# Kernel optimization log

Measured on AMD Instinct MI355X. Metric: run time of the kernel, lower is better.

## Reference

```python
import jax, jax.numpy as jnp
import numpy as np

D = 1024
H = 16
HD = D // H
B = 8
S = 1024


def setup_inputs() -> dict:
    key = jax.random.key(0)
    ks = jax.random.split(key, 12)
    std = 0.02
    inp = {
        "x": jax.random.normal(ks[0], (B, S, D), jnp.float32),
        "rel_pos_enc": jax.random.normal(ks[1], (S, HD), jnp.float32) * std,
        "attention_mask": jax.random.randint(ks[2], (B, S), 0, 2, jnp.int32),
        "Wq": jax.random.normal(ks[3], (D, D), jnp.float32) * std,
        "bq": jnp.zeros((D,), jnp.float32),
        "Wk": jax.random.normal(ks[4], (D, D), jnp.float32) * std,
        "bk": jnp.zeros((D,), jnp.float32),
        "Wv": jax.random.normal(ks[5], (D, D), jnp.float32) * std,
        "bv": jnp.zeros((D,), jnp.float32),
        "Wo": jax.random.normal(ks[6], (D, D), jnp.float32) * std,
        "bo": jnp.zeros((D,), jnp.float32),
    }
    return inp


def reference(x, rel_pos_enc, attention_mask, Wq, bq, Wk, bk, Wv, bv, Wo, bo):
    b, s, d = x.shape
    scale = HD ** -0.5
    # projections + split heads -> [B, H, S, hd]
    q = (x @ Wq + bq).reshape(b, s, H, HD).transpose(0, 2, 1, 3)
    k = (x @ Wk + bk).reshape(b, s, H, HD).transpose(0, 2, 1, 3)
    v = (x @ Wv + bv).reshape(b, s, H, HD).transpose(0, 2, 1, 3)
    # content scores [B,H,S,S]
    scores = jnp.einsum("bhsd,bhtd->bhst", q, k) * scale
    # additive relative-position bias: q . rel_pos_enc[t]  -> [B,H,S,S]
    scores = scores + jnp.einsum("bhsd,td->bhst", q, rel_pos_enc)
    # key-padding mask [B,S] -> [B,1,1,S]
    scores = jnp.where(attention_mask[:, None, None, :] == 0, -jnp.inf, scores)
    attn = jax.nn.softmax(scores, axis=-1)
    ctx = jnp.einsum("bhst,bhtd->bhsd", attn, v)
    ctx = ctx.transpose(0, 2, 1, 3).reshape(b, s, d)
    return ctx @ Wo + bo
```

## Files before the change

kernel.cpp:

```cpp
#include <hip/hip_runtime.h>

#define DD 1024
#define HH 16
#define HDD 64
#define BBATCH 8
#define SS 1024
#define NROW (BBATCH*SS)
#define PSTR 72

typedef _Float16 f16x8 __attribute__((ext_vector_type(8)));
typedef _Float16 f16x4 __attribute__((ext_vector_type(4)));
typedef float    f32x4 __attribute__((ext_vector_type(4)));

__device__ __forceinline__ void async_cp16(const void* g, void* l) {
    __builtin_amdgcn_global_load_lds(
        (const __attribute__((address_space(1))) void*)g,
        (__attribute__((address_space(3))) void*)l, 16, 0, 0);
}

__global__ __launch_bounds__(256) void conv_x_kernel(
    const float* __restrict__ x, _Float16* __restrict__ xh)
{
    size_t i8 = ((size_t)blockIdx.x * 256 + threadIdx.x) * 8;
    float4 v0 = *(const float4*)&x[i8];
    float4 v1 = *(const float4*)&x[i8 + 4];
    float vf[8] = {v0.x, v0.y, v0.z, v0.w, v1.x, v1.y, v1.z, v1.w};
    f16x8 hv;
    #pragma unroll
    for (int c = 0; c < 8; c++) hv[c] = (_Float16)vf[c];
    *(f16x8*)&xh[i8] = hv;
}

__global__ __launch_bounds__(256) void conv_w_kernel(
    const float* __restrict__ Wq, const float* __restrict__ Wk,
    const float* __restrict__ Wv, const float* __restrict__ Wo,
    _Float16* __restrict__ wt, _Float16* __restrict__ wot)
{
    __shared__ float T[64][65];
    const int z = blockIdx.z;
    const float* src = (z == 0) ? Wq : (z == 1) ? Wk : (z == 2) ? Wv : Wo;
    _Float16* dh = (z < 3) ? wt + (size_t)z * 1024 * 1024 : wot;
    const int k0 = blockIdx.x * 64, n0 = blockIdx.y * 64;
    const int tid = threadIdx.x;

    #pragma unroll
    for (int rep = 0; rep < 4; rep++) {
        int e = rep * 256 + tid;
        int kr = e >> 4, nc = (e & 15) * 4;
        *(float4*)&T[kr][nc] = *(const float4*)&src[(size_t)(k0 + kr) * 1024 + n0 + nc];
    }
    __syncthreads();
    #pragma unroll
    for (int rep = 0; rep < 4; rep++) {
        int e = rep * 256 + tid;
        int nr = e >> 4, kc = (e & 15) * 4;
        f16x4 hv;
        #pragma unroll
        for (int c = 0; c < 4; c++) hv[c] = (_Float16)T[kc + c][nr];
        *(f16x4*)&dh[(size_t)(n0 + nr) * 1024 + k0 + kc] = hv;
    }
}

__global__ __launch_bounds__(256) void gemm_f16(
    const _Float16* __restrict__ Ag, const _Float16* __restrict__ Bg,
    const float* __restrict__ b0, const float* __restrict__ b1,
    const float* __restrict__ b2, const float* __restrict__ rel,
    _Float16* __restrict__ oq, _Float16* __restrict__ okh,
    _Float16* __restrict__ ovt, float* __restrict__ dOut, int mode)
{
    __shared__ _Float16 smem[32768];

    const int tid = threadIdx.x;
    const int w = tid >> 6, l = tid & 63;
    const int lane15 = l & 15, quad = l >> 4;
    const int rm = (w >> 1) * 64, cn = (w & 1) * 64;
    const size_t r0 = (size_t)blockIdx.y * 128;
    const size_t n0 = (size_t)blockIdx.x * 128;

    const int srow = tid >> 3;
    const int schp = tid & 7;
    const int sch  = schp ^ (srow & 7);

    f32x4 acc[4][4] = {};

    #pragma unroll
    for (int i = 0; i < 4; i++) {
        int row = i * 32 + srow;
        int s = row * 8 + schp;
        async_cp16(&Ag[(r0 + row) * 1024 + sch * 8], &smem[s * 8]);
        async_cp16(&Bg[(n0 + row) * 1024 + sch * 8], &smem[8192 + s * 8]);
    }
    #pragma unroll
    for (int i = 0; i < 4; i++) {
        int row = i * 32 + srow;
        int s = row * 8 + schp;
        async_cp16(&Ag[(r0 + row) * 1024 + 64 + sch * 8], &smem[16384 + s * 8]);
        async_cp16(&Bg[(n0 + row) * 1024 + 64 + sch * 8], &smem[16384 + 8192 + s * 8]);
    }

    for (int ks = 0; ks < 16; ks++) {
        const _Float16* Ah = smem + (ks & 1) * 16384;
        const _Float16* Bh = Ah + 8192;

        if (ks < 15) asm volatile("s_waitcnt vmcnt(8)" ::: "memory");
        else         asm volatile("s_waitcnt vmcnt(0)" ::: "memory");
        __builtin_amdgcn_sched_barrier(0);
        __builtin_amdgcn_s_barrier();
        __builtin_amdgcn_sched_barrier(0);

        #pragma unroll
        for (int ksub = 0; ksub < 2; ksub++) {
            f16x8 ah[4], bh4[4];
            #pragma unroll
            for (int ii = 0; ii < 4; ii++) {
                int row = rm + ii * 16 + lane15;
                int chp = (ksub * 4 + quad) ^ (row & 7);
                ah[ii] = *(const f16x8*)&Ah[row * 64 + chp * 8];
            }
            #pragma unroll
            for (int jj = 0; jj < 4; jj++) {
                int col = cn + jj * 16 + lane15;
                int chp = (ksub * 4 + quad) ^ (col & 7);
                bh4[jj] = *(const f16x8*)&Bh[col * 64 + chp * 8];
            }
            #pragma unroll
            for (int ii = 0; ii < 4; ii++)
                #pragma unroll
                for (int jj = 0; jj < 4; jj++)
                    acc[ii][jj] = __builtin_amdgcn_mfma_f32_16x16x32_f16(
                        ah[ii], bh4[jj], acc[ii][jj], 0, 0, 0);
        }

        __builtin_amdgcn_sched_barrier(0);
        __builtin_amdgcn_s_barrier();
        __builtin_amdgcn_sched_barrier(0);

        if (ks + 2 < 16) {
            const int kb = (ks + 2) * 64;
            _Float16* An = smem + (ks & 1) * 16384;
            _Float16* Bn = An + 8192;
            #pragma unroll
            for (int i = 0; i < 4; i++) {
                int row = i * 32 + srow;
                int s = row * 8 + schp;
                async_cp16(&Ag[(r0 + row) * 1024 + kb + sch * 8], &An[s * 8]);
                async_cp16(&Bg[(n0 + row) * 1024 + kb + sch * 8], &Bn[s * 8]);
            }
        }
    }

    if (mode == 0) {
        const int z = blockIdx.x >> 3;
        const float* bias = (z == 0) ? b0 : (z == 1) ? b1 : b2;
        const int nbase = (blockIdx.x & 7) * 128 + cn;
        #pragma unroll
        for (int ii = 0; ii < 4; ii++)
            #pragma unroll
            for (int jj = 0; jj < 4; jj++) {
                int nc = nbase + jj * 16 + lane15;
                int hh = nc >> 6, hd = nc & 63;
                float bsv = bias[nc];
                #pragma unroll
                for (int r = 0; r < 4; r++) {
                    int gr = (int)r0 + rm + ii * 16 + quad * 4 + r;
                    int bb = gr >> 10, s = gr & 1023;
                    float val = acc[ii][jj][r] + bsv;
                    size_t hidx = (((size_t)bb * HH + hh) * SS + s) * HDD + hd;
                    if (z == 0) {
                        oq[hidx] = (_Float16)val;
                    } else if (z == 1) {
                        okh[hidx] = (_Float16)(val * 0.125f + rel[s * HDD + hd]);
                    } else {
                        ovt[(((size_t)bb * HH + hh) * HDD + hd) * SS + s] = (_Float16)val;
                    }
                }
            }
    } else {
        #pragma unroll
        for (int ii = 0; ii < 4; ii++)
            #pragma unroll
            for (int jj = 0; jj < 4; jj++) {
                int nc = (int)n0 + cn + jj * 16 + lane15;
                float bsv = b0[nc];
                #pragma unroll
                for (int r = 0; r < 4; r++) {
                    int gr = (int)r0 + rm + ii * 16 + quad * 4 + r;
                    dOut[(size_t)gr * DD + nc] = acc[ii][jj][r] + bsv;
                }
            }
    }
}

__global__ __launch_bounds__(512, 4) void attn_mfma(
    const _Float16* __restrict__ qh, const _Float16* __restrict__ kh,
    const _Float16* __restrict__ vt, const int* __restrict__ mask,
    _Float16* __restrict__ ctx)
{
    __shared__ _Float16 Kbuf[2][64 * PSTR];
    __shared__ _Float16 Vbuf[2][64 * PSTR];
    __shared__ _Float16 Ps[128 * PSTR];
    __shared__ float maddL[1024];

    const int tid = threadIdx.x;
    const int w = tid >> 6, l = tid & 63;
    const int lane15 = l & 15, quad = l >> 4;
    const int id = blockIdx.x;
    const int qt = id >> 7;
    const int bh = id & 127;
    const int b = bh >> 4, h = bh & 15;
    const size_t kbase0 = (size_t)bh * SS;
    const size_t vbase0 = (size_t)bh * HDD;
    const int qrow_blk = qt * 128 + w * 16;

    for (int i = tid; i < 1024; i += 512)
        maddL[i] = (mask[b * SS + i] == 0) ? -1e30f : 0.0f;

    f16x8 qf[2];
    #pragma unroll
    for (int ks = 0; ks < 2; ks++)
        qf[ks] = *(const f16x8*)&qh[(kbase0 + qrow_blk + lane15) * HDD + ks * 32 + quad * 8];

    f16x8 vone;
    #pragma unroll
    for (int j = 0; j < 8; j++) vone[j] = (lane15 == 0) ? (_Float16)1.0f : (_Float16)0.0f;

    f32x4 O[5] = {};

    const int grow = tid >> 3;
    const int gcc  = (tid & 7) * 8;
    const _Float16* kp = &kh[(kbase0 + grow) * HDD + gcc];
    const _Float16* vp = &vt[(vbase0 + grow) * SS + gcc];
    f16x8 kreg = *(const f16x8*)kp;
    f16x8 vreg = *(const f16x8*)vp;

    int p = 0;
    for (int kt = 0; kt < 16; kt++) {
        *(f16x8*)&Kbuf[p][grow * PSTR + gcc] = kreg;
        *(f16x8*)&Vbuf[p][grow * PSTR + gcc] = vreg;
        __syncthreads();

        const int nkt = (kt + 1) & 15;
        kreg = *(const f16x8*)(kp + (size_t)nkt * 64 * HDD);
        vreg = *(const f16x8*)(vp + (size_t)nkt * 64);

        const int t0 = kt * 64;

        f32x4 S[4];
        #pragma unroll
        for (int nt = 0; nt < 4; nt++) {
            f16x8 kf0 = *(const f16x8*)&Kbuf[p][(nt * 16 + lane15) * PSTR + quad * 8];
            f16x8 kf1 = *(const f16x8*)&Kbuf[p][(nt * 16 + lane15) * PSTR + 32 + quad * 8];
            f32x4 c = {};
            c = __builtin_amdgcn_mfma_f32_16x16x32_f16(qf[0], kf0, c, 0, 0, 0);
            c = __builtin_amdgcn_mfma_f32_16x16x32_f16(qf[1], kf1, c, 0, 0, 0);
            S[nt] = c;
        }

        const int rowb = w * 16 + quad * 4;
        #pragma unroll
        for (int nt = 0; nt < 4; nt++) {
            float madd = maddL[t0 + nt * 16 + lane15] - 3.0f;
            int colp = (nt * 16 + lane15 + 16 * quad) & 63;
            #pragma unroll
            for (int r = 0; r < 4; r++)
                Ps[(rowb + r) * PSTR + colp] = (_Float16)__expf(S[nt][r] + madd);
        }

        const int swz = 16 * (lane15 >> 2);
        #pragma unroll
        for (int ks2 = 0; ks2 < 2; ks2++) {
            int colp = (ks2 * 32 + quad * 8 + swz) & 63;
            f16x8 pf = *(const f16x8*)&Ps[(w * 16 + lane15) * PSTR + colp];
            #pragma unroll
            for (int nd = 0; nd < 4; nd++) {
                f16x8 vf = *(const f16x8*)&Vbuf[p][(nd * 16 + lane15) * PSTR + ks2 * 32 + quad * 8];
                O[nd] = __builtin_amdgcn_mfma_f32_16x16x32_f16(pf, vf, O[nd], 0, 0, 0);
            }
            O[4] = __builtin_amdgcn_mfma_f32_16x16x32_f16(pf, vone, O[4], 0, 0, 0);
        }
        p ^= 1;
    }

    float linv[4];
    #pragma unroll
    for (int r = 0; r < 4; r++) {
        float lsum = __shfl(O[4][r], l & 48, 64);
        linv[r] = 1.0f / lsum;
    }
    #pragma unroll
    for (int nd = 0; nd < 4; nd++) {
        int d = nd * 16 + lane15;
        #pragma unroll
        for (int r = 0; r < 4; r++) {
            int qrow = qt * 128 + w * 16 + quad * 4 + r;
            ctx[((size_t)b * SS + qrow) * DD + h * HDD + d] =
                (_Float16)(O[nd][r] * linv[r]);
        }
    }
}

extern "C" void kernel_launch(void* const* d_in, const int* in_sizes, int n_in,
                              void* d_out, int out_size, void* d_ws, size_t ws_size,
                              hipStream_t stream) {
    const float* x    = (const float*)d_in[0];
    const float* rel  = (const float*)d_in[1];
    const int*   mask = (const int*)d_in[2];
    const float* Wq = (const float*)d_in[3];  const float* bq = (const float*)d_in[4];
    const float* Wk = (const float*)d_in[5];  const float* bk = (const float*)d_in[6];
    const float* Wv = (const float*)d_in[7];  const float* bv = (const float*)d_in[8];
    const float* Wo = (const float*)d_in[9];  const float* bo = (const float*)d_in[10];
    float* out = (float*)d_out;

    const size_t XN = (size_t)NROW * DD;
    char* p = (char*)d_ws;
    _Float16* xh  = (_Float16*)p; p += XN * 2;
    _Float16* wt  = (_Float16*)p; p += (size_t)3072 * 1024 * 2;
    _Float16* wot = (_Float16*)p; p += (size_t)1024 * 1024 * 2;
    _Float16* qhp = (_Float16*)p; p += XN * 2;
    _Float16* khp = (_Float16*)p; p += XN * 2;
    _Float16* vtp = (_Float16*)p; p += XN * 2;
    _Float16* ctx = xh;

    conv_x_kernel<<<dim3((unsigned)(XN / 2048)), 256, 0, stream>>>(x, xh);
    conv_w_kernel<<<dim3(16, 16, 4), 256, 0, stream>>>(Wq, Wk, Wv, Wo, wt, wot);
    gemm_f16<<<dim3(24, 64), 256, 0, stream>>>(
        xh, wt, bq, bk, bv, rel, qhp, khp, vtp, nullptr, 0);
    attn_mfma<<<dim3(1024), 512, 0, stream>>>(
        qhp, khp, vtp, mask, ctx);
    gemm_f16<<<dim3(8, 64), 256, 0, stream>>>(
        ctx, wot, bo, nullptr, nullptr, nullptr,
        nullptr, nullptr, nullptr, out, 1);
}
```

Baseline: 289.7 us.

## Load K/V fragments directly from global memory and remap GEMM workgroups across XCDs

The attention kernel drops its shared-memory double-buffered K/V staging and per-tile barriers, so each wave reads its MFMA operand fragments straight from global memory and relies on L2/cache for reuse across the 8 waves. The GEMM remaps workgroup IDs so consecutive tiles land on the same XCD chunk, which is meant to improve L2 locality. This removes barrier and LDS traffic but multiplies global or L2 loads per block and exposes load latency that the prefetch used to hide. A barrier is added after the mask fill.

After: 450.3 us. +55.4%, slower.

```diff
diff --git a/kernel.cpp b/kernel.cpp
--- a/kernel.cpp
+++ b/kernel.cpp
@@ -74,8 +74,16 @@
     const int w = tid >> 6, l = tid & 63;
     const int lane15 = l & 15, quad = l >> 4;
     const int rm = (w >> 1) * 64, cn = (w & 1) * 64;
-    const size_t r0 = (size_t)blockIdx.y * 128;
-    const size_t n0 = (size_t)blockIdx.x * 128;
+
+    const int nwg = (int)(gridDim.x * gridDim.y);
+    const int chunk = nwg >> 3;
+    const int orig = (int)(blockIdx.y * gridDim.x + blockIdx.x);
+    const int wgid = (orig & 7) * chunk + (orig >> 3);
+    const int bx = wgid % (int)gridDim.x;
+    const int by = wgid / (int)gridDim.x;
+
+    const size_t r0 = (size_t)by * 128;
+    const size_t n0 = (size_t)bx * 128;
 
     const int srow = tid >> 3;
     const int schp = tid & 7;
@@ -150,9 +158,9 @@
     }
 
     if (mode == 0) {
-        const int z = blockIdx.x >> 3;
+        const int z = bx >> 3;
         const float* bias = (z == 0) ? b0 : (z == 1) ? b1 : b2;
-        const int nbase = (blockIdx.x & 7) * 128 + cn;
+        const int nbase = (bx & 7) * 128 + cn;
         #pragma unroll
         for (int ii = 0; ii < 4; ii++)
             #pragma unroll
@@ -196,8 +204,6 @@
     const _Float16* __restrict__ vt, const int* __restrict__ mask,
     _Float16* __restrict__ ctx)
 {
-    __shared__ _Float16 Kbuf[2][64 * PSTR];
-    __shared__ _Float16 Vbuf[2][64 * PSTR];
     __shared__ _Float16 Ps[128 * PSTR];
     __shared__ float maddL[1024];
 
@@ -214,6 +220,7 @@
 
     for (int i = tid; i < 1024; i += 512)
         maddL[i] = (mask[b * SS + i] == 0) ? -1e30f : 0.0f;
+    __syncthreads();
 
     f16x8 qf[2];
     #pragma unroll
@@ -226,30 +233,18 @@
 
     f32x4 O[5] = {};
 
-    const int grow = tid >> 3;
-    const int gcc  = (tid & 7) * 8;
-    const _Float16* kp = &kh[(kbase0 + grow) * HDD + gcc];
-    const _Float16* vp = &vt[(vbase0 + grow) * SS + gcc];
-    f16x8 kreg = *(const f16x8*)kp;
-    f16x8 vreg = *(const f16x8*)vp;
-
-    int p = 0;
+    const _Float16* kfrag = &kh[(kbase0 + lane15) * HDD + quad * 8];
+    const _Float16* vfrag = &vt[(vbase0 + lane15) * SS + quad * 8];
+
     for (int kt = 0; kt < 16; kt++) {
-        *(f16x8*)&Kbuf[p][grow * PSTR + gcc] = kreg;
-        *(f16x8*)&Vbuf[p][grow * PSTR + gcc] = vreg;
-        __syncthreads();
-
-        const int nkt = (kt + 1) & 15;
-        kreg = *(const f16x8*)(kp + (size_t)nkt * 64 * HDD);
-        vreg = *(const f16x8*)(vp + (size_t)nkt * 64);
-
         const int t0 = kt * 64;
 
         f32x4 S[4];
         #pragma unroll
         for (int nt = 0; nt < 4; nt++) {
-            f16x8 kf0 = *(const f16x8*)&Kbuf[p][(nt * 16 + lane15) * PSTR + quad * 8];
-            f16x8 kf1 = *(const f16x8*)&Kbuf[p][(nt * 16 + lane15) * PSTR + 32 + quad * 8];
+            const _Float16* kp = kfrag + (size_t)(t0 + nt * 16) * HDD;
+            f16x8 kf0 = *(const f16x8*)kp;
+            f16x8 kf1 = *(const f16x8*)(kp + 32);
             f32x4 c = {};
             c = __builtin_amdgcn_mfma_f32_16x16x32_f16(qf[0], kf0, c, 0, 0, 0);
             c = __builtin_amdgcn_mfma_f32_16x16x32_f16(qf[1], kf1, c, 0, 0, 0);
@@ -273,12 +268,11 @@
             f16x8 pf = *(const f16x8*)&Ps[(w * 16 + lane15) * PSTR + colp];
             #pragma unroll
             for (int nd = 0; nd < 4; nd++) {
-                f16x8 vf = *(const f16x8*)&Vbuf[p][(nd * 16 + lane15) * PSTR + ks2 * 32 + quad * 8];
+                f16x8 vf = *(const f16x8*)(vfrag + (size_t)(nd * 16) * SS + t0 + ks2 * 32);
                 O[nd] = __builtin_amdgcn_mfma_f32_16x16x32_f16(pf, vf, O[nd], 0, 0, 0);
             }
             O[4] = __builtin_amdgcn_mfma_f32_16x16x32_f16(pf, vone, O[4], 0, 0, 0);
         }
-        p ^= 1;
     }
 
     float linv[4];
```

## Process two query row groups per wave to reuse K/V tiles in attention

Applied to the files above, without the earlier changes.

Each wave now handles 32 query rows (two 16-row groups) instead of 16, so each block covers 256 query rows and the grid is halved to 512 blocks. K and V tiles loaded into shared memory, and the K/V fragments read from it, are reused across both row groups, which halves global and LDS traffic for K/V per query. The cost is more registers for the doubled accumulators, a larger P buffer in shared memory, and fewer blocks to fill the GPU.

Result: faster. 277.9 us (-4.1%).

```diff
diff --git a/kernel.cpp b/kernel.cpp
--- a/kernel.cpp
+++ b/kernel.cpp
@@ -198,7 +198,7 @@
 {
     __shared__ _Float16 Kbuf[2][64 * PSTR];
     __shared__ _Float16 Vbuf[2][64 * PSTR];
-    __shared__ _Float16 Ps[128 * PSTR];
+    __shared__ _Float16 Ps[256 * PSTR];
     __shared__ float maddL[1024];
 
     const int tid = threadIdx.x;
@@ -210,21 +210,23 @@
     const int b = bh >> 4, h = bh & 15;
     const size_t kbase0 = (size_t)bh * SS;
     const size_t vbase0 = (size_t)bh * HDD;
-    const int qrow_blk = qt * 128 + w * 16;
+    const int qrow_blk = qt * 256 + w * 32;
 
     for (int i = tid; i < 1024; i += 512)
         maddL[i] = (mask[b * SS + i] == 0) ? -1e30f : 0.0f;
 
-    f16x8 qf[2];
-    #pragma unroll
-    for (int ks = 0; ks < 2; ks++)
-        qf[ks] = *(const f16x8*)&qh[(kbase0 + qrow_blk + lane15) * HDD + ks * 32 + quad * 8];
+    f16x8 qf[2][2];
+    #pragma unroll
+    for (int g = 0; g < 2; g++)
+        #pragma unroll
+        for (int ks = 0; ks < 2; ks++)
+            qf[g][ks] = *(const f16x8*)&qh[(kbase0 + qrow_blk + g * 16 + lane15) * HDD + ks * 32 + quad * 8];
 
     f16x8 vone;
     #pragma unroll
     for (int j = 0; j < 8; j++) vone[j] = (lane15 == 0) ? (_Float16)1.0f : (_Float16)0.0f;
 
-    f32x4 O[5] = {};
+    f32x4 O[2][5] = {};
 
     const int grow = tid >> 3;
     const int gcc  = (tid & 7) * 8;
@@ -245,56 +247,59 @@
 
         const int t0 = kt * 64;
 
-        f32x4 S[4];
         #pragma unroll
         for (int nt = 0; nt < 4; nt++) {
             f16x8 kf0 = *(const f16x8*)&Kbuf[p][(nt * 16 + lane15) * PSTR + quad * 8];
             f16x8 kf1 = *(const f16x8*)&Kbuf[p][(nt * 16 + lane15) * PSTR + 32 + quad * 8];
-            f32x4 c = {};
-            c = __builtin_amdgcn_mfma_f32_16x16x32_f16(qf[0], kf0, c, 0, 0, 0);
-            c = __builtin_amdgcn_mfma_f32_16x16x32_f16(qf[1], kf1, c, 0, 0, 0);
-            S[nt] = c;
-        }
-
-        const int rowb = w * 16 + quad * 4;
-        #pragma unroll
-        for (int nt = 0; nt < 4; nt++) {
             float madd = maddL[t0 + nt * 16 + lane15] - 3.0f;
             int colp = (nt * 16 + lane15 + 16 * quad) & 63;
             #pragma unroll
-            for (int r = 0; r < 4; r++)
-                Ps[(rowb + r) * PSTR + colp] = (_Float16)__expf(S[nt][r] + madd);
+            for (int g = 0; g < 2; g++) {
+                f32x4 c = {};
+                c = __builtin_amdgcn_mfma_f32_16x16x32_f16(qf[g][0], kf0, c, 0, 0, 0);
+                c = __builtin_amdgcn_mfma_f32_16x16x32_f16(qf[g][1], kf1, c, 0, 0, 0);
+                int rowb = w * 32 + g * 16 + quad * 4;
+                #pragma unroll
+                for (int r = 0; r < 4; r++)
+                    Ps[(rowb + r) * PSTR + colp] = (_Float16)__expf(c[r] + madd);
+            }
         }
 
         const int swz = 16 * (lane15 >> 2);
         #pragma unroll
         for (int ks2 = 0; ks2 < 2; ks2++) {
             int colp = (ks2 * 32 + quad * 8 + swz) & 63;
-            f16x8 pf = *(const f16x8*)&Ps[(w * 16 + lane15) * PSTR + colp];
+            f16x8 pf0 = *(const f16x8*)&Ps[(w * 32 + lane15) * PSTR + colp];
+            f16x8 pf1 = *(const f16x8*)&Ps[(w * 32 + 16 + lane15) * PSTR + colp];
             #pragma unroll
             for (int nd = 0; nd < 4; nd++) {
                 f16x8 vf = *(const f16x8*)&Vbuf[p][(nd * 16 + lane15) * PSTR + ks2 * 32 + quad * 8];
-                O[nd] = __builtin_amdgcn_mfma_f32_16x16x32_f16(pf, vf, O[nd], 0, 0, 0);
-            }
-            O[4] = __builtin_amdgcn_mfma_f32_16x16x32_f16(pf, vone, O[4], 0, 0, 0);
+                O[0][nd] = __builtin_amdgcn_mfma_f32_16x16x32_f16(pf0, vf, O[0][nd], 0, 0, 0);
+                O[1][nd] = __builtin_amdgcn_mfma_f32_16x16x32_f16(pf1, vf, O[1][nd], 0, 0, 0);
+            }
+            O[0][4] = __builtin_amdgcn_mfma_f32_16x16x32_f16(pf0, vone, O[0][4], 0, 0, 0);
+            O[1][4] = __builtin_amdgcn_mfma_f32_16x16x32_f16(pf1, vone, O[1][4], 0, 0, 0);
         }
         p ^= 1;
     }
 
-    float linv[4];
-    #pragma unroll
-    for (int r = 0; r < 4; r++) {
-        float lsum = __shfl(O[4][r], l & 48, 64);
-        linv[r] = 1.0f / lsum;
-    }
-    #pragma unroll
-    for (int nd = 0; nd < 4; nd++) {
-        int d = nd * 16 + lane15;
+    #pragma unroll
+    for (int g = 0; g < 2; g++) {
+        float linv[4];
         #pragma unroll
         for (int r = 0; r < 4; r++) {
-            int qrow = qt * 128 + w * 16 + quad * 4 + r;
-            ctx[((size_t)b * SS + qrow) * DD + h * HDD + d] =
-                (_Float16)(O[nd][r] * linv[r]);
+            float lsum = __shfl(O[g][4][r], l & 48, 64);
+            linv[r] = 1.0f / lsum;
+        }
+        #pragma unroll
+        for (int nd = 0; nd < 4; nd++) {
+            int d = nd * 16 + lane15;
+            #pragma unroll
+            for (int r = 0; r < 4; r++) {
+                int qrow = qt * 256 + w * 32 + g * 16 + quad * 4 + r;
+                ctx[((size_t)b * SS + qrow) * DD + h * HDD + d] =
+                    (_Float16)(O[g][nd][r] * linv[r]);
+            }
         }
     }
 }
@@ -325,7 +330,7 @@
     conv_w_kernel<<<dim3(16, 16, 4), 256, 0, stream>>>(Wq, Wk, Wv, Wo, wt, wot);
     gemm_f16<<<dim3(24, 64), 256, 0, stream>>>(
         xh, wt, bq, bk, bv, rel, qhp, khp, vtp, nullptr, 0);
-    attn_mfma<<<dim3(1024), 512, 0, stream>>>(
+    attn_mfma<<<dim3(512), 512, 0, stream>>>(
         qhp, khp, vtp, mask, ctx);
     gemm_f16<<<dim3(8, 64), 256, 0, stream>>>(
         ctx, wot, bo, nullptr, nullptr, nullptr,
```

## Switch attention to 32x32 MFMA with register-resident P and 256-row query tiles

Applied to the files above, without the earlier changes.

The attention kernel now computes S transposed (K·Q) with 32x32x16 MFMA so the probability tile stays in registers. It is repacked across lane halves with shuffles instead of being round-tripped through shared memory. Row sums are accumulated in registers instead of through an extra MFMA against a ones vector, and the mask becomes a multiplicative fp16 array. Each block now handles 256 query rows with 32 rows per wave, halving the grid to 512 blocks, which raises register pressure and lowers the number of blocks per CU.

Result: faster. 280.5 us (-3.2%).

```diff
diff --git a/kernel.cpp b/kernel.cpp
--- a/kernel.cpp
+++ b/kernel.cpp
@@ -11,6 +11,8 @@
 typedef _Float16 f16x8 __attribute__((ext_vector_type(8)));
 typedef _Float16 f16x4 __attribute__((ext_vector_type(4)));
 typedef float    f32x4 __attribute__((ext_vector_type(4)));
+typedef float    f32x16 __attribute__((ext_vector_type(16)));
+typedef unsigned int u32x4 __attribute__((ext_vector_type(4)));
 
 __device__ __forceinline__ void async_cp16(const void* g, void* l) {
     __builtin_amdgcn_global_load_lds(
@@ -198,33 +200,30 @@
 {
     __shared__ _Float16 Kbuf[2][64 * PSTR];
     __shared__ _Float16 Vbuf[2][64 * PSTR];
-    __shared__ _Float16 Ps[128 * PSTR];
-    __shared__ float maddL[1024];
+    __shared__ _Float16 maskh[1024];
 
     const int tid = threadIdx.x;
     const int w = tid >> 6, l = tid & 63;
-    const int lane15 = l & 15, quad = l >> 4;
+    const int l31 = l & 31, hi = l >> 5;
     const int id = blockIdx.x;
     const int qt = id >> 7;
     const int bh = id & 127;
     const int b = bh >> 4, h = bh & 15;
     const size_t kbase0 = (size_t)bh * SS;
     const size_t vbase0 = (size_t)bh * HDD;
-    const int qrow_blk = qt * 128 + w * 16;
+    const int qbase = qt * 256 + w * 32;
 
     for (int i = tid; i < 1024; i += 512)
-        maddL[i] = (mask[b * SS + i] == 0) ? -1e30f : 0.0f;
-
-    f16x8 qf[2];
-    #pragma unroll
-    for (int ks = 0; ks < 2; ks++)
-        qf[ks] = *(const f16x8*)&qh[(kbase0 + qrow_blk + lane15) * HDD + ks * 32 + quad * 8];
-
-    f16x8 vone;
-    #pragma unroll
-    for (int j = 0; j < 8; j++) vone[j] = (lane15 == 0) ? (_Float16)1.0f : (_Float16)0.0f;
-
-    f32x4 O[5] = {};
+        maskh[i] = (_Float16)(mask[b * SS + i] != 0 ? 1.0f : 0.0f);
+
+    f16x8 qfrag[4];
+    #pragma unroll
+    for (int kc = 0; kc < 4; kc++)
+        qfrag[kc] = *(const f16x8*)&qh[(kbase0 + qbase + l31) * HDD + kc * 16 + hi * 8];
+
+    f32x16 O0 = {};
+    f32x16 O1 = {};
+    float rs = 0.0f;
 
     const int grow = tid >> 3;
     const int gcc  = (tid & 7) * 8;
@@ -233,10 +232,10 @@
     f16x8 kreg = *(const f16x8*)kp;
     f16x8 vreg = *(const f16x8*)vp;
 
-    int p = 0;
+    int pb = 0;
     for (int kt = 0; kt < 16; kt++) {
-        *(f16x8*)&Kbuf[p][grow * PSTR + gcc] = kreg;
-        *(f16x8*)&Vbuf[p][grow * PSTR + gcc] = vreg;
+        *(f16x8*)&Kbuf[pb][grow * PSTR + gcc] = kreg;
+        *(f16x8*)&Vbuf[pb][grow * PSTR + gcc] = vreg;
         __syncthreads();
 
         const int nkt = (kt + 1) & 15;
@@ -245,57 +244,65 @@
 
         const int t0 = kt * 64;
 
-        f32x4 S[4];
-        #pragma unroll
-        for (int nt = 0; nt < 4; nt++) {
-            f16x8 kf0 = *(const f16x8*)&Kbuf[p][(nt * 16 + lane15) * PSTR + quad * 8];
-            f16x8 kf1 = *(const f16x8*)&Kbuf[p][(nt * 16 + lane15) * PSTR + 32 + quad * 8];
-            f32x4 c = {};
-            c = __builtin_amdgcn_mfma_f32_16x16x32_f16(qf[0], kf0, c, 0, 0, 0);
-            c = __builtin_amdgcn_mfma_f32_16x16x32_f16(qf[1], kf1, c, 0, 0, 0);
-            S[nt] = c;
+        #pragma unroll
+        for (int T = 0; T < 2; T++) {
+            f32x16 S = {};
+            #pragma unroll
+            for (int kc = 0; kc < 4; kc++) {
+                f16x8 kf = *(const f16x8*)&Kbuf[pb][(T * 32 + l31) * PSTR + kc * 16 + hi * 8];
+                S = __builtin_amdgcn_mfma_f32_32x32x16_f16(kf, qfrag[kc], S, 0, 0, 0);
+            }
+
+            unsigned short phb[16];
+            #pragma unroll
+            for (int rq = 0; rq < 4; rq++) {
+                f16x4 mh = *(const f16x4*)&maskh[t0 + T * 32 + rq * 8 + hi * 4];
+                #pragma unroll
+                for (int dd = 0; dd < 4; dd++) {
+                    const int r = rq * 4 + dd;
+                    float e = __expf(S[r] - 3.0f) * (float)mh[dd];
+                    _Float16 eh = (_Float16)e;
+                    rs += (float)eh;
+                    phb[r] = *(unsigned short*)&eh;
+                }
+            }
+            unsigned pk[8];
+            #pragma unroll
+            for (int c = 0; c < 8; c++)
+                pk[c] = (unsigned)phb[2 * c] | ((unsigned)phb[2 * c + 1] << 16);
+
+            #pragma unroll
+            for (int ct = 0; ct < 2; ct++) {
+                unsigned s0 = hi ? pk[4 * ct + 0] : pk[4 * ct + 2];
+                unsigned s1 = hi ? pk[4 * ct + 1] : pk[4 * ct + 3];
+                unsigned r0 = (unsigned)__shfl_xor((int)s0, 32, 64);
+                unsigned r1 = (unsigned)__shfl_xor((int)s1, 32, 64);
+                u32x4 W;
+                W[0] = hi ? r0 : pk[4 * ct + 0];
+                W[1] = hi ? r1 : pk[4 * ct + 1];
+                W[2] = hi ? pk[4 * ct + 2] : r0;
+                W[3] = hi ? pk[4 * ct + 3] : r1;
+                f16x8 pf = __builtin_bit_cast(f16x8, W);
+
+                f16x8 vf0 = *(const f16x8*)&Vbuf[pb][(l31) * PSTR + T * 32 + ct * 16 + hi * 8];
+                O0 = __builtin_amdgcn_mfma_f32_32x32x16_f16(pf, vf0, O0, 0, 0, 0);
+                f16x8 vf1 = *(const f16x8*)&Vbuf[pb][(32 + l31) * PSTR + T * 32 + ct * 16 + hi * 8];
+                O1 = __builtin_amdgcn_mfma_f32_32x32x16_f16(pf, vf1, O1, 0, 0, 0);
+            }
         }
-
-        const int rowb = w * 16 + quad * 4;
-        #pragma unroll
-        for (int nt = 0; nt < 4; nt++) {
-            float madd = maddL[t0 + nt * 16 + lane15] - 3.0f;
-            int colp = (nt * 16 + lane15 + 16 * quad) & 63;
-            #pragma unroll
-            for (int r = 0; r < 4; r++)
-                Ps[(rowb + r) * PSTR + colp] = (_Float16)__expf(S[nt][r] + madd);
-        }
-
-        const int swz = 16 * (lane15 >> 2);
-        #pragma unroll
-        for (int ks2 = 0; ks2 < 2; ks2++) {
-            int colp = (ks2 * 32 + quad * 8 + swz) & 63;
-            f16x8 pf = *(const f16x8*)&Ps[(w * 16 + lane15) * PSTR + colp];
-            #pragma unroll
-            for (int nd = 0; nd < 4; nd++) {
-                f16x8 vf = *(const f16x8*)&Vbuf[p][(nd * 16 + lane15) * PSTR + ks2 * 32 + quad * 8];
-                O[nd] = __builtin_amdgcn_mfma_f32_16x16x32_f16(pf, vf, O[nd], 0, 0, 0);
-            }
-            O[4] = __builtin_amdgcn_mfma_f32_16x16x32_f16(pf, vone, O[4], 0, 0, 0);
-        }
-        p ^= 1;
-    }
-
-    float linv[4];
-    #pragma unroll
-    for (int r = 0; r < 4; r++) {
-        float lsum = __shfl(O[4][r], l & 48, 64);
-        linv[r] = 1.0f / lsum;
-    }
-    #pragma unroll
-    for (int nd = 0; nd < 4; nd++) {
-        int d = nd * 16 + lane15;
-        #pragma unroll
-        for (int r = 0; r < 4; r++) {
-            int qrow = qt * 128 + w * 16 + quad * 4 + r;
-            ctx[((size_t)b * SS + qrow) * DD + h * HDD + d] =
-                (_Float16)(O[nd][r] * linv[r]);
-        }
+        pb ^= 1;
+    }
+
+    rs += __shfl_xor(rs, 32, 64);
+    float linv = 1.0f / rs;
+
+    #pragma unroll
+    for (int r = 0; r < 16; r++) {
+        int q = (r & 3) + 8 * (r >> 2) + 4 * hi;
+        float lv = __shfl(linv, q, 64);
+        size_t rowoff = ((size_t)b * SS + qbase + q) * DD + h * HDD;
+        ctx[rowoff + l31]      = (_Float16)(O0[r] * lv);
+        ctx[rowoff + 32 + l31] = (_Float16)(O1[r] * lv);
     }
 }
 
@@ -325,7 +332,7 @@
     conv_w_kernel<<<dim3(16, 16, 4), 256, 0, stream>>>(Wq, Wk, Wv, Wo, wt, wot);
     gemm_f16<<<dim3(24, 64), 256, 0, stream>>>(
         xh, wt, bq, bk, bv, rel, qhp, khp, vtp, nullptr, 0);
-    attn_mfma<<<dim3(1024), 512, 0, stream>>>(
+    attn_mfma<<<dim3(512), 512, 0, stream>>>(
         qhp, khp, vtp, mask, ctx);
     gemm_f16<<<dim3(8, 64), 256, 0, stream>>>(
         ctx, wot, bo, nullptr, nullptr, nullptr,
```
